# Performance work log

Hardware: AMD Instinct MI355X
Metric: run time of the kernel (lower is better)

Reference implementation:

```python
import jax, jax.numpy as jnp
import numpy as np

NTOKENS = 100000
NHID = 512
TPC = 317                      # ntokens_per_class
NCLASSES = int(np.ceil(NTOKENS / TPC))  # 316
BATCH = 2048


def setup_inputs() -> dict:
    key = jax.random.key(0)
    k1, k2, k3, k4 = jax.random.split(key, 4)
    initrange = 0.1
    inputs = jax.random.normal(k1, (BATCH, NHID), dtype=jnp.float32)
    labels = jax.random.randint(k2, (BATCH,), 0, NTOKENS, dtype=jnp.int64)
    layer_top_W = jax.random.uniform(k3, (NHID, NCLASSES), minval=-initrange, maxval=initrange, dtype=jnp.float32)
    layer_top_b = jnp.zeros((NCLASSES,), dtype=jnp.float32)
    layer_bottom_W = jax.random.uniform(k4, (NCLASSES, NHID, TPC), minval=-initrange, maxval=initrange, dtype=jnp.float32)
    layer_bottom_b = jnp.zeros((NCLASSES, TPC), dtype=jnp.float32)
    return {
        "inputs": inputs,
        "labels": labels,
        "ntokens_per_class": TPC,
        "layer_top_W": layer_top_W,
        "layer_top_b": layer_top_b,
        "layer_bottom_W": layer_bottom_W,
        "layer_bottom_b": layer_bottom_b,
    }


def reference(inputs, labels, ntokens_per_class, layer_top_W, layer_top_b,
              layer_bottom_W, layer_bottom_b):
    batch_size = inputs.shape[0]
    tpc = ntokens_per_class

    # top layer: [B, nclasses]
    top_logits = inputs @ layer_top_W + layer_top_b
    top_probs = jax.nn.softmax(top_logits, axis=1)

    pos_top = labels // tpc          # [B] class index
    pos_bot = labels % tpc           # [B] within-class index

    # gather per-sample bottom weights: [B, nhid, tpc], then tiny bmm
    Wg = layer_bottom_W[pos_top]
    bg = layer_bottom_b[pos_top]
    bottom_logits = jnp.einsum('bd,bdt->bt', inputs, Wg) + bg
    bottom_probs = jax.nn.softmax(bottom_logits, axis=1)

    ar = jnp.arange(batch_size)
    target_probs = top_probs[ar, pos_top] * bottom_probs[ar, pos_bot]

    top_indx = jnp.argmax(top_probs, axis=1)
    bottom_indx = jnp.argmax(bottom_probs, axis=1)
    real_indx = top_indx * tpc + bottom_indx

    loss = -jnp.mean(jnp.log(target_probs))

    # preds: outer product of top and bottom probs, flattened: [B, nclasses*tpc]
    preds = (top_probs[:, :, None] * bottom_probs[:, None, :]).reshape(batch_size, -1)

    return (loss, target_probs, top_probs, bottom_probs, top_indx, bottom_indx, real_indx, preds)
```

## Files before the change

### kernel.cpp

```cpp
#include <hip/hip_runtime.h>
#include <hip/hip_bf16.h>
#include <cmath>

#define B    2048
#define NH   512
#define NC   316
#define TPC  317
#define ROWLEN (NC * TPC)

#define OFF_LOSS    ((size_t)0)
#define OFF_TGT     ((size_t)1)
#define OFF_TOPP    ((size_t)(1 + B))
#define OFF_BOTP    (OFF_TOPP + (size_t)B * NC)
#define OFF_TIDX    (OFF_BOTP + (size_t)B * TPC)
#define OFF_BIDX    (OFF_TIDX + (size_t)B)
#define OFF_RIDX    (OFF_BIDX + (size_t)B)
#define OFF_PREDS   (OFF_RIDX + (size_t)B)

#define K1_SB 8

__global__ __launch_bounds__(320) void k_top(const float* __restrict__ X,
                                             const float* __restrict__ Wt,
                                             const float* __restrict__ bt,
                                             float* __restrict__ out) {
    __shared__ float xs[K1_SB][NH];
    __shared__ float lg[K1_SB][NC];
    const int tid = threadIdx.x;
    const int b0 = blockIdx.x * K1_SB;

    for (int idx = tid; idx < K1_SB * NH; idx += 320) {
        xs[idx >> 9][idx & (NH - 1)] = X[(size_t)(b0 + (idx >> 9)) * NH + (idx & (NH - 1))];
    }
    __syncthreads();

    if (tid < NC) {
        float acc[K1_SB];
        #pragma unroll
        for (int s = 0; s < K1_SB; ++s) acc[s] = 0.f;
        #pragma unroll 2
        for (int k = 0; k < NH; k += 4) {
            const float w0 = Wt[(k + 0) * NC + tid];
            const float w1 = Wt[(k + 1) * NC + tid];
            const float w2 = Wt[(k + 2) * NC + tid];
            const float w3 = Wt[(k + 3) * NC + tid];
            #pragma unroll
            for (int s = 0; s < K1_SB; ++s) {
                const float4 x4 = *(const float4*)&xs[s][k];
                acc[s] += x4.x * w0 + x4.y * w1 + x4.z * w2 + x4.w * w3;
            }
        }
        const float bbv = bt[tid];
        #pragma unroll
        for (int s = 0; s < K1_SB; ++s) lg[s][tid] = acc[s] + bbv;
    }
    __syncthreads();

    const int wave = tid >> 6, lane = tid & 63;
    float* __restrict__ top_probs = out + OFF_TOPP;
    float* __restrict__ top_indx  = out + OFF_TIDX;

    for (int s = wave; s < K1_SB; s += 5) {
        const int b = b0 + s;
        float m = -INFINITY; int mi = 0;
        for (int c = lane; c < NC; c += 64) {
            float v = lg[s][c];
            if (v > m) { m = v; mi = c; }
        }
        for (int off = 32; off > 0; off >>= 1) {
            float om = __shfl_xor(m, off);
            int omi  = __shfl_xor(mi, off);
            if (om > m || (om == m && omi < mi)) { m = om; mi = omi; }
        }
        float sum = 0.f;
        for (int c = lane; c < NC; c += 64) sum += expf(lg[s][c] - m);
        for (int off = 32; off > 0; off >>= 1) sum += __shfl_xor(sum, off);
        const float inv = 1.0f / sum;
        for (int c = lane; c < NC; c += 64)
            top_probs[(size_t)b * NC + c] = expf(lg[s][c] - m) * inv;
        if (lane == 0) top_indx[b] = (float)mi;
    }
}

#define KCH     8
#define KLEN    (NH / KCH)
#define SG      8
#define SCR_PAD 320

__global__ __launch_bounds__(320) void k_blogits(const float* __restrict__ X,
                                                 const int* __restrict__ labels,
                                                 const float* __restrict__ Wb,
                                                 float* __restrict__ scratch) {
    __shared__ int   list[B];
    __shared__ float xs[SG][KLEN];
    __shared__ int   cnt;

    const int tid = threadIdx.x;
    const int c   = blockIdx.x;
    const int kc  = blockIdx.y;
    if (tid == 0) cnt = 0;
    __syncthreads();

    for (int i = tid; i < B; i += 320) {
        int lab = labels[i];
        if (lab / TPC == c) list[atomicAdd(&cnt, 1)] = i;
    }
    __syncthreads();
    const int n = cnt;
    if (n == 0) return;

    const float* __restrict__ Wc = Wb + (size_t)c * NH * TPC + (size_t)kc * KLEN * TPC;
    const float* __restrict__ Xc = X + kc * KLEN;

    for (int start = 0; start < n; start += SG) {
        const int ns = min(SG, n - start);
        __syncthreads();
        for (int idx = tid; idx < ns * KLEN; idx += 320) {
            xs[idx >> 6][idx & (KLEN - 1)] =
                Xc[(size_t)list[start + (idx >> 6)] * NH + (idx & (KLEN - 1))];
        }
        __syncthreads();

        if (tid < TPC) {
            float acc[SG];
            #pragma unroll
            for (int s = 0; s < SG; ++s) acc[s] = 0.f;
            #pragma unroll 2
            for (int k = 0; k < KLEN; k += 4) {
                const float w0 = Wc[(size_t)(k + 0) * TPC + tid];
                const float w1 = Wc[(size_t)(k + 1) * TPC + tid];
                const float w2 = Wc[(size_t)(k + 2) * TPC + tid];
                const float w3 = Wc[(size_t)(k + 3) * TPC + tid];
                #pragma unroll
                for (int s = 0; s < SG; ++s) {
                    const float4 x4 = *(const float4*)&xs[s][k];
                    acc[s] += x4.x * w0 + x4.y * w1 + x4.z * w2 + x4.w * w3;
                }
            }
            for (int s = 0; s < ns; ++s)
                scratch[((size_t)list[start + s] * KCH + kc) * SCR_PAD + tid] = acc[s];
        }
    }
}

__global__ __launch_bounds__(256) void k_bfinal(const int* __restrict__ labels,
                                                const float* __restrict__ bbias,
                                                const float* __restrict__ scratch,
                                                float* __restrict__ out) {
    const int tid  = threadIdx.x;
    const int lane = tid & 63;
    const int b    = blockIdx.x * 4 + (tid >> 6);

    const int lab = labels[b];
    const int c   = lab / TPC;
    const int pb  = lab - c * TPC;

    float lgv[5];
    #pragma unroll
    for (int i = 0; i < 5; ++i) {
        const int t = lane + 64 * i;
        float v = -INFINITY;
        if (t < TPC) {
            v = bbias[(size_t)c * TPC + t];
            #pragma unroll
            for (int kc = 0; kc < KCH; ++kc)
                v += scratch[((size_t)b * KCH + kc) * SCR_PAD + t];
        }
        lgv[i] = v;
    }

    float m = -INFINITY; int mi = 0;
    #pragma unroll
    for (int i = 0; i < 5; ++i) {
        const int t = lane + 64 * i;
        if (lgv[i] > m) { m = lgv[i]; mi = t; }
    }
    for (int off = 32; off > 0; off >>= 1) {
        float om = __shfl_xor(m, off);
        int omi  = __shfl_xor(mi, off);
        if (om > m || (om == m && omi < mi)) { m = om; mi = omi; }
    }

    float pv[5];
    float sum = 0.f;
    #pragma unroll
    for (int i = 0; i < 5; ++i) {
        const int t = lane + 64 * i;
        pv[i] = (t < TPC) ? expf(lgv[i] - m) : 0.f;
        sum += pv[i];
    }
    for (int off = 32; off > 0; off >>= 1) sum += __shfl_xor(sum, off);
    const float inv = 1.0f / sum;

    float* __restrict__ bot = out + OFF_BOTP + (size_t)b * TPC;
    float tsel = 0.f;
    #pragma unroll
    for (int i = 0; i < 5; ++i) {
        const int t = lane + 64 * i;
        if (t < TPC) {
            const float p = pv[i] * inv;
            bot[t] = p;
            if (t == pb) tsel = p;
        }
    }
    for (int off = 32; off > 0; off >>= 1) tsel += __shfl_xor(tsel, off);

    if (lane == 0) {
        out[OFF_TGT + b]  = out[OFF_TOPP + (size_t)b * NC + c] * tsel;
        out[OFF_BIDX + b] = (float)mi;
        out[OFF_RIDX + b] = out[OFF_TIDX + b] * (float)TPC + (float)mi;
    }
}

#define K3_THREADS 256
#define K3_ITERS   20
#define K3_BLOCKS_PER_ROW ((ROWLEN + K3_THREADS * K3_ITERS - 1) / (K3_THREADS * K3_ITERS))

__global__ __launch_bounds__(K3_THREADS) void k_preds(const float* __restrict__ out_ro,
                                                      float* __restrict__ preds) {
    __shared__ float tp[NC];
    __shared__ float bp[TPC];
    const int b = blockIdx.y;
    const int tid = threadIdx.x;

    const float* __restrict__ trow = out_ro + OFF_TOPP + (size_t)b * NC;
    const float* __restrict__ brow = out_ro + OFF_BOTP + (size_t)b * TPC;
    for (int i = tid; i < NC;  i += K3_THREADS) tp[i] = trow[i];
    for (int i = tid; i < TPC; i += K3_THREADS) bp[i] = brow[i];
    __syncthreads();

    int j = blockIdx.x * (K3_THREADS * K3_ITERS) + tid;
    int c = j / TPC;
    int t = j - c * TPC;
    float* __restrict__ row = preds + (size_t)b * ROWLEN;

    #pragma unroll
    for (int i = 0; i < K3_ITERS; ++i) {
        if (j < ROWLEN) row[j] = tp[c] * bp[t];
        j += K3_THREADS;
        t += K3_THREADS;
        if (t >= TPC) { t -= TPC; c++; }
    }
}

__global__ __launch_bounds__(256) void k_loss(const float* __restrict__ out_ro,
                                              float* __restrict__ out) {
    __shared__ float red[4];
    const int tid = threadIdx.x;
    const float* __restrict__ target = out_ro + OFF_TGT;
    float s = 0.f;
    for (int i = tid; i < B; i += 256) s += logf(target[i]);
    for (int off = 32; off > 0; off >>= 1) s += __shfl_xor(s, off);
    if ((tid & 63) == 0) red[tid >> 6] = s;
    __syncthreads();
    if (tid == 0) {
        float tot = red[0] + red[1] + red[2] + red[3];
        out[OFF_LOSS] = -tot / (float)B;
    }
}

extern "C" void kernel_launch(void* const* d_in, const int* in_sizes, int n_in,
                              void* d_out, int out_size, void* d_ws, size_t ws_size,
                              hipStream_t stream) {
    const float* X      = (const float*)d_in[0];
    const int*   labels = (const int*)d_in[1];
    const float* Wt = (const float*)d_in[3];
    const float* bt = (const float*)d_in[4];
    const float* Wb = (const float*)d_in[5];
    const float* bb = (const float*)d_in[6];
    float* out = (float*)d_out;
    float* scratch = out + OFF_PREDS;

    k_blogits<<<dim3(NC, KCH), dim3(320), 0, stream>>>(X, labels, Wb, scratch);
    k_top<<<dim3(B / K1_SB), dim3(320), 0, stream>>>(X, Wt, bt, out);
    k_bfinal<<<dim3(B / 4), dim3(256), 0, stream>>>(labels, bb, scratch, out);
    k_preds<<<dim3(K3_BLOCKS_PER_ROW, B), dim3(K3_THREADS), 0, stream>>>(out, out + OFF_PREDS);
    k_loss<<<dim3(1), dim3(256), 0, stream>>>(out, out);
}
```

Before: 385.8 us.

## Read X directly via uniform scalar addresses instead of LDS staging; widen sample group

Both the top-logit and bottom-logit kernels stop staging input rows in shared memory and instead read them with wave-uniform addresses (readfirstlane), so the loads can go through the scalar/constant cache path. This removes the LDS fill loops and the barriers between sample groups in k_blogits. The sample group size doubles from 8 to 16, and the list is padded with duplicate indices so full groups can be computed unconditionally. The cost is more registers per thread and more global/cache traffic for X.

New measurement: 365.1 us. 5.4% less time.

```diff
diff --git a/kernel.cpp b/kernel.cpp
--- a/kernel.cpp
+++ b/kernel.cpp
@@ -23,20 +23,15 @@
                                              const float* __restrict__ Wt,
                                              const float* __restrict__ bt,
                                              float* __restrict__ out) {
-    __shared__ float xs[K1_SB][NH];
     __shared__ float lg[K1_SB][NC];
     const int tid = threadIdx.x;
     const int b0 = blockIdx.x * K1_SB;
-
-    for (int idx = tid; idx < K1_SB * NH; idx += 320) {
-        xs[idx >> 9][idx & (NH - 1)] = X[(size_t)(b0 + (idx >> 9)) * NH + (idx & (NH - 1))];
-    }
-    __syncthreads();
 
     if (tid < NC) {
         float acc[K1_SB];
         #pragma unroll
         for (int s = 0; s < K1_SB; ++s) acc[s] = 0.f;
+        const float* __restrict__ Xb = X + (size_t)b0 * NH;
         #pragma unroll 2
         for (int k = 0; k < NH; k += 4) {
             const float w0 = Wt[(k + 0) * NC + tid];
@@ -45,8 +40,8 @@
             const float w3 = Wt[(k + 3) * NC + tid];
             #pragma unroll
             for (int s = 0; s < K1_SB; ++s) {
-                const float4 x4 = *(const float4*)&xs[s][k];
-                acc[s] += x4.x * w0 + x4.y * w1 + x4.z * w2 + x4.w * w3;
+                const float4 xv = *(const float4*)&Xb[s * NH + k];
+                acc[s] += xv.x * w0 + xv.y * w1 + xv.z * w2 + xv.w * w3;
             }
         }
         const float bbv = bt[tid];
@@ -83,16 +78,15 @@
 
 #define KCH     8
 #define KLEN    (NH / KCH)
-#define SG      8
+#define SG      16
 #define SCR_PAD 320
 
 __global__ __launch_bounds__(320) void k_blogits(const float* __restrict__ X,
                                                  const int* __restrict__ labels,
                                                  const float* __restrict__ Wb,
                                                  float* __restrict__ scratch) {
-    __shared__ int   list[B];
-    __shared__ float xs[SG][KLEN];
-    __shared__ int   cnt;
+    __shared__ int list[B + SG];
+    __shared__ int cnt;
 
     const int tid = threadIdx.x;
     const int c   = blockIdx.x;
@@ -107,33 +101,38 @@
     __syncthreads();
     const int n = cnt;
     if (n == 0) return;
+    if (tid < SG) list[n + tid] = list[0];
+    __syncthreads();
 
     const float* __restrict__ Wc = Wb + (size_t)c * NH * TPC + (size_t)kc * KLEN * TPC;
-    const float* __restrict__ Xc = X + kc * KLEN;
+    const int xoff = kc * KLEN;
 
     for (int start = 0; start < n; start += SG) {
         const int ns = min(SG, n - start);
-        __syncthreads();
-        for (int idx = tid; idx < ns * KLEN; idx += 320) {
-            xs[idx >> 6][idx & (KLEN - 1)] =
-                Xc[(size_t)list[start + (idx >> 6)] * NH + (idx & (KLEN - 1))];
-        }
-        __syncthreads();
+        int sb[SG];
+        #pragma unroll
+        for (int s = 0; s < SG; ++s)
+            sb[s] = __builtin_amdgcn_readfirstlane(list[start + s]) * NH + xoff;
 
         if (tid < TPC) {
             float acc[SG];
             #pragma unroll
             for (int s = 0; s < SG; ++s) acc[s] = 0.f;
-            #pragma unroll 2
+
             for (int k = 0; k < KLEN; k += 4) {
                 const float w0 = Wc[(size_t)(k + 0) * TPC + tid];
                 const float w1 = Wc[(size_t)(k + 1) * TPC + tid];
                 const float w2 = Wc[(size_t)(k + 2) * TPC + tid];
                 const float w3 = Wc[(size_t)(k + 3) * TPC + tid];
                 #pragma unroll
-                for (int s = 0; s < SG; ++s) {
-                    const float4 x4 = *(const float4*)&xs[s][k];
-                    acc[s] += x4.x * w0 + x4.y * w1 + x4.z * w2 + x4.w * w3;
+                for (int s = 0; s < 8; ++s) {
+                    const float4 xv = *(const float4*)&X[sb[s] + k];
+                    acc[s] += xv.x * w0 + xv.y * w1 + xv.z * w2 + xv.w * w3;
+                }
+                #pragma unroll
+                for (int s = 8; s < SG; ++s) {
+                    const float4 xv = *(const float4*)&X[sb[s] + k];
+                    acc[s] += xv.x * w0 + xv.y * w1 + xv.z * w2 + xv.w * w3;
                 }
             }
             for (int s = 0; s < ns; ++s)
```
